# Kernel optimization log

Measured on AMD Instinct MI355X. Metric: run time of the kernel, lower is better.

## Reference

```python
import jax, jax.numpy as jnp
import numpy as np

RES = (128, 128)       # frequency modes (fx, fy)
T = (1.0, 1.0)         # period per dimension
J = 2                  # simplex dimension (polygon)
B = 2                  # batch size
NV = 512               # num vertices = num elements (polygon ring)


def setup_inputs() -> dict:
    key = jax.random.key(0)
    V = jax.random.uniform(key, (B, NV, 2), dtype=jnp.float32)
    idx = jnp.arange(NV, dtype=jnp.int32)
    # polygon ring connectivity: edge i = (i, i+1 mod NV)
    E = jnp.broadcast_to(jnp.stack([idx, (idx + 1) % NV], axis=-1)[None], (B, NV, 2))
    D = jnp.ones((B, NV, 1), jnp.float32)
    return {"V": V, "E": E, "D": D}


def _omega():
    # freq_init='fft': integer fft/rfft frequencies, scaled by 2*pi/t per dim
    f0 = np.fft.fftfreq(RES[0], d=1.0 / RES[0])
    f1 = np.fft.rfftfreq(RES[1], d=1.0 / RES[1])
    om = np.stack(np.meshgrid(f0, f1, indexing='ij'), axis=-1).astype(np.float32)
    om[..., 0] *= 2.0 * np.pi / T[0]
    om[..., 1] *= 2.0 * np.pi / T[1]
    return jnp.asarray(om)  # (fx, fy//2+1, 2)


def reference(V, E, D):
    b, nv, nd = V.shape
    # subdim: append auxiliary origin vertex, turn edges into triangles
    Vaux = jnp.concatenate([V, jnp.zeros((b, 1, nd), V.dtype)], axis=1)
    Eaux = jnp.concatenate([E, jnp.full((b, E.shape[1], 1), nv, E.dtype)], axis=-1)
    P = jax.vmap(lambda v, e: v[e])(Vaux, Eaux)           # (B, ne, j+1, 2)
    # C = j! * signed simplex content = det of edge vectors (2x2)
    Vs = P[:, :, :J, :] - P[:, :, J:J + 1, :]
    C = (Vs[:, :, 0, 0] * Vs[:, :, 1, 1] - Vs[:, :, 0, 1] * Vs[:, :, 1, 0])[..., None]  # (B, ne, 1)
    omega = _omega()
    sig = jnp.einsum('bejd,xyd->bejxy', P, omega)         # (B, ne, 3, fx, fy2)
    esig = jnp.stack([jnp.cos(sig), -jnp.sin(sig)], axis=-1)  # (B, ne, 3, fx, fy2, 2)
    # divided-difference denominator: prod over circular shifts 1..j
    d1 = sig - sig[:, :, jnp.array([1, 2, 0])]
    d2 = sig - sig[:, :, jnp.array([2, 0, 1])]
    denom = d1 * d2
    zero = denom == 0
    tmp = jnp.sum(esig / jnp.where(zero, 1.0, denom)[..., None], axis=2)  # (B, ne, fx, fy2, 2)
    tmp = jnp.where(jnp.any(zero, axis=2)[..., None], 0.0, tmp)
    CD = C * D                                            # (B, ne, nch=1)
    F = jnp.einsum('bexyr,bec->bxycr', tmp, CD)           # (B, fx, fy2, 1, 2)
    # DC component: -1/j! * sum(C*D)
    dc = -jnp.sum(CD, axis=1) / 2.0                       # (B, 1)
    F = F.at[:, 0, 0].set(dc[..., None])
    F = -F                                                # img(F, deg=j=2): multiply by i^2 = -1
    F = F * (RES[0] ** J)                                 # density-preserving normalization
    return F
```

## Files before the change

kernel.cpp:

```cpp
#include <hip/hip_runtime.h>
#include <math.h>


#define NVERT 512
#define RESX  128
#define RESY2 65
#define BATCH 2
#define NKX   8
#define NCH   32
#define ELEN  (NVERT / NCH)

typedef float f2 __attribute__((ext_vector_type(2)));

__device__ __forceinline__ float sig1(float x, float y, float omx, float omy) {
#pragma clang fp contract(off)
  float p = x * omx;
  float q = y * omy;
  return p + q;
}

__device__ __forceinline__ f2 sig2(f2 x, f2 y, float omx, float omy) {
#pragma clang fp contract(off)
  f2 p = x * omx;
  f2 q = y * omy;
  return p + q;
}

extern "C" __global__ __launch_bounds__(256, 8)
void ddsl_spec(const float* __restrict__ V, const float* __restrict__ D,
               float* __restrict__ out) {
  const int tx = threadIdx.x;
  const int ty = threadIdx.y;
  const int ky = blockIdx.x;
  const int b  = blockIdx.y;
  const int z  = blockIdx.z;

  __shared__ float sVx[NVERT];
  __shared__ float sVy[NVERT];
  __shared__ __align__(8) float sCD[NVERT];
  __shared__ float red[2][NCH][NKX];
  __shared__ float sDCv;

  const int tid = ty * NKX + tx;

  {
    const float2* Vb = (const float2*)(V + b * (NVERT * 2));
    for (int i = tid; i < NVERT; i += 256) {
      const int j = (i + 1) & (NVERT - 1);
      float2 v0 = Vb[i];
      float2 v1 = Vb[j];
      sVx[i] = v0.x;
      sVy[i] = v0.y;
      sCD[i] = (v0.x * v1.y - v0.y * v1.x) * D[b * NVERT + i];
    }
  }
  __syncthreads();

  const int kx = z * NKX + tx;
  const float kxf = (float)((kx < 64) ? kx : kx - 128);
  const float kyf = (float)ky;
  const float TWO_PI = 6.2831854820251465f;
  const float INV2PI = 0.15915493667125702f;
  const float omx = TWO_PI * kxf;
  const float omy = TWO_PI * kyf;

  const int e0 = ty * ELEN;

  float sP = sig1(sVx[e0], sVy[e0], omx, omy);
  float rfP = __builtin_amdgcn_fractf(sP * INV2PI);
  float cP  = __builtin_amdgcn_cosf(rfP);
  float snP = __builtin_amdgcn_sinf(rfP);

  f2 accRe = {0.0f, 0.0f};
  f2 accIm = {0.0f, 0.0f};

#pragma unroll 4
  for (int t = 0; t < ELEN / 2; ++t) {
    const int e = e0 + 2 * t;
    const int j1 = (e + 1) & (NVERT - 1);
    const int j2 = (e + 2) & (NVERT - 1);
    f2 xx = {sVx[j1], sVx[j2]};
    f2 yy = {sVy[j1], sVy[j2]};
    f2 cd = *(const f2*)&sCD[e];

    f2 sN = sig2(xx, yy, omx, omy);
    f2 rf = sN * INV2PI;
    float rf0 = __builtin_amdgcn_fractf(rf.x);
    float rf1 = __builtin_amdgcn_fractf(rf.y);
    f2 cN  = {__builtin_amdgcn_cosf(rf0), __builtin_amdgcn_cosf(rf1)};
    f2 snN = {__builtin_amdgcn_sinf(rf0), __builtin_amdgcn_sinf(rf1)};

    f2 s0  = {sP, sN.x};
    f2 c0  = {cP, cN.x};
    f2 sn0 = {snP, snN.x};
    f2 d01 = s0 - sN;
    f2 prod = s0 * sN * d01;
    float i0 = (fabsf(prod.x) < 1e-30f) ? 0.0f : __builtin_amdgcn_rcpf(prod.x);
    float i1 = (fabsf(prod.y) < 1e-30f) ? 0.0f : __builtin_amdgcn_rcpf(prod.y);
    f2 inv = {i0, i1};

    f2 tre = __builtin_elementwise_fma(c0, sN,
             __builtin_elementwise_fma(-cN, s0, d01));
    f2 tim = __builtin_elementwise_fma(snN, s0, -(sn0 * sN));
    f2 w = cd * inv;

    accRe = __builtin_elementwise_fma(w, tre, accRe);
    accIm = __builtin_elementwise_fma(w, tim, accIm);

    sP = sN.y; cP = cN.y; snP = snN.y;
  }

  red[0][ty][tx] = accRe.x + accRe.y;
  red[1][ty][tx] = accIm.x + accIm.y;
  __syncthreads();

  if (ky == 0 && z == 0 && tid >= 128 && tid < 192) {
    const int lane = tid - 128;
    float s = 0.0f;
#pragma unroll
    for (int k = 0; k < NVERT / 64; ++k) s += sCD[lane + 64 * k];
    for (int off = 32; off > 0; off >>= 1) s += __shfl_down(s, off, 64);
    if (lane == 0) sDCv = 8192.0f * s;
  }
  __syncthreads();

  if (ty < 2) {
    float s = 0.0f;
#pragma unroll
    for (int k = 0; k < NCH; ++k) s += red[ty][k][tx];
    float val = -16384.0f * s;
    if (ky == 0 && z == 0 && tx == 0) val = sDCv;
    out[b * (RESX * RESY2 * 2) + kx * (RESY2 * 2) + ky * 2 + ty] = val;
  }
}

extern "C" void kernel_launch(void* const* d_in, const int* in_sizes, int n_in,
                              void* d_out, int out_size, void* d_ws, size_t ws_size,
                              hipStream_t stream) {
  (void)in_sizes; (void)n_in; (void)d_ws; (void)ws_size; (void)out_size;
  const float* V = (const float*)d_in[0];
  const float* D = (const float*)d_in[2];
  float* out = (float*)d_out;

  dim3 grid(RESY2, BATCH, 16);
  dim3 block(NKX, NCH, 1);
  ddsl_spec<<<grid, block, 0, stream>>>(V, D, out);
}
```

Before: 63.64 us.

## Pad shared vertex arrays to avoid bank conflicts and merge DC reduction sync

```diff
diff --git a/kernel.cpp b/kernel.cpp
--- a/kernel.cpp
+++ b/kernel.cpp
@@ -11,6 +11,8 @@
 #define ELEN  (NVERT / NCH)
 
 typedef float f2 __attribute__((ext_vector_type(2)));
+
+#define SW(v) ((v) + ((v) >> 3))
 
 __device__ __forceinline__ float sig1(float x, float y, float omx, float omy) {
 #pragma clang fp contract(off)
@@ -35,9 +37,9 @@
   const int b  = blockIdx.y;
   const int z  = blockIdx.z;
 
-  __shared__ float sVx[NVERT];
-  __shared__ float sVy[NVERT];
-  __shared__ __align__(8) float sCD[NVERT];
+  __shared__ float sVx[SW(NVERT) + 4];
+  __shared__ float sVy[SW(NVERT) + 4];
+  __shared__ float sCD[SW(NVERT) + 4];
   __shared__ float red[2][NCH][NKX];
   __shared__ float sDCv;
 
@@ -45,16 +47,35 @@
 
   {
     const float2* Vb = (const float2*)(V + b * (NVERT * 2));
-    for (int i = tid; i < NVERT; i += 256) {
+#pragma unroll
+    for (int k = 0; k < 2; ++k) {
+      const int i = tid + 256 * k;
       const int j = (i + 1) & (NVERT - 1);
       float2 v0 = Vb[i];
       float2 v1 = Vb[j];
-      sVx[i] = v0.x;
-      sVy[i] = v0.y;
-      sCD[i] = (v0.x * v1.y - v0.y * v1.x) * D[b * NVERT + i];
+      const int w = SW(i);
+      sVx[w] = v0.x;
+      sVy[w] = v0.y;
+      sCD[w] = (v0.x * v1.y - v0.y * v1.x) * D[b * NVERT + i];
+      if (i == 0) {
+        sVx[SW(NVERT)] = v0.x;
+        sVy[SW(NVERT)] = v0.y;
+      }
     }
   }
   __syncthreads();
+
+  if (ky == 0 && z == 0 && tid >= 128 && tid < 192) {
+    const int lane = tid - 128;
+    float s = 0.0f;
+#pragma unroll
+    for (int k = 0; k < NVERT / 64; ++k) {
+      const int idx = lane + 64 * k;
+      s += sCD[SW(idx)];
+    }
+    for (int off = 32; off > 0; off >>= 1) s += __shfl_down(s, off, 64);
+    if (lane == 0) sDCv = 8192.0f * s;
+  }
 
   const int kx = z * NKX + tx;
   const float kxf = (float)((kx < 64) ? kx : kx - 128);
@@ -65,8 +86,9 @@
   const float omy = TWO_PI * kyf;
 
   const int e0 = ty * ELEN;
+  const int wb = SW(e0);
 
-  float sP = sig1(sVx[e0], sVy[e0], omx, omy);
+  float sP = sig1(sVx[wb], sVy[wb], omx, omy);
   float rfP = __builtin_amdgcn_fractf(sP * INV2PI);
   float cP  = __builtin_amdgcn_cosf(rfP);
   float snP = __builtin_amdgcn_sinf(rfP);
@@ -74,14 +96,18 @@
   f2 accRe = {0.0f, 0.0f};
   f2 accIm = {0.0f, 0.0f};
 
-#pragma unroll 4
+#pragma unroll
   for (int t = 0; t < ELEN / 2; ++t) {
-    const int e = e0 + 2 * t;
-    const int j1 = (e + 1) & (NVERT - 1);
-    const int j2 = (e + 2) & (NVERT - 1);
-    f2 xx = {sVx[j1], sVx[j2]};
-    f2 yy = {sVy[j1], sVy[j2]};
-    f2 cd = *(const f2*)&sCD[e];
+    const int c1 = 2 * t + 1;
+    const int c2 = 2 * t + 2;
+    const int ce = 2 * t;
+    const int o1 = c1 + (c1 >> 3);
+    const int o2 = c2 + (c2 >> 3);
+    const int oe = ce + (ce >> 3);
+
+    f2 xx = {sVx[wb + o1], sVx[wb + o2]};
+    f2 yy = {sVy[wb + o1], sVy[wb + o2]};
+    f2 cd = {sCD[wb + oe], sCD[wb + o1]};
 
     f2 sN = sig2(xx, yy, omx, omy);
     f2 rf = sN * INV2PI;
@@ -114,16 +140,6 @@
   red[1][ty][tx] = accIm.x + accIm.y;
   __syncthreads();
 
-  if (ky == 0 && z == 0 && tid >= 128 && tid < 192) {
-    const int lane = tid - 128;
-    float s = 0.0f;
-#pragma unroll
-    for (int k = 0; k < NVERT / 64; ++k) s += sCD[lane + 64 * k];
-    for (int off = 32; off > 0; off >>= 1) s += __shfl_down(s, off, 64);
-    if (lane == 0) sDCv = 8192.0f * s;
-  }
-  __syncthreads();
-
   if (ty < 2) {
     float s = 0.0f;
 #pragma unroll
```

New measurement: 63.58 us. About the same (-0.1%).
